# Kernel tuning notes

Hardware: AMD Instinct MI355X
Metric: run time of the kernel (lower is better)

The kernel has to match this reference:

```python
import jax, jax.numpy as jnp
import numpy as np

T, B = 512, 64
I, H, A, O = 256, 1024, 128, 1024  # input, hidden, adapt, output sizes


def _lstm_cell(x, h, c, wih, whh, bih, bhh):
    # standard torch nn.LSTMCell, gate order i,f,g,o
    g = x @ wih.T + bih + h @ whh.T + bhh
    i, f, gg, o = jnp.split(g, 4, axis=1)
    i = jax.nn.sigmoid(i)
    f = jax.nn.sigmoid(f)
    gg = jnp.tanh(gg)
    o = jax.nn.sigmoid(o)
    c2 = f * c + i * gg
    return o * jnp.tanh(c2), c2


def _alstm_cell(x, h, c, wih, whh, b, adapt, ninp, nhid):
    # adapt chunks: [ninp, nhid, 4*nhid, 4*nhid, 4*nhid]
    splits = [ninp, ninp + nhid, ninp + nhid + 4 * nhid, ninp + nhid + 8 * nhid]
    a_x, a_h, a_ig, a_hg, a_b = jnp.split(adapt, splits, axis=1)
    igates = ((x * a_x) @ wih.T) * a_ig + b * a_b
    hgates = ((h * a_h) @ whh.T) * a_hg
    g = igates + hgates
    i, f, gg, o = jnp.split(g, 4, axis=1)
    i = jax.nn.sigmoid(i)
    f = jax.nn.sigmoid(f)
    gg = jnp.tanh(gg)
    o = jax.nn.sigmoid(o)
    c2 = f * c + i * gg
    return o * jnp.tanh(c2), c2


def setup_inputs() -> dict:
    key = jax.random.key(0)
    ks = jax.random.split(key, 20)
    n = lambda k, *s: jax.random.normal(k, s, dtype=jnp.float32) * 0.05
    psz0 = I + 13 * H          # layer0 policy size
    psz1 = H + 13 * O          # layer1 policy size
    return {
        "x": jax.random.normal(ks[0], (T, B, I), dtype=jnp.float32),
        # layer 0 adapt LSTMCell: input = A + I + H
        "a_wih0": n(ks[1], 4 * A, A + I + H), "a_whh0": n(ks[2], 4 * A, A),
        "a_bih0": n(ks[3], 4 * A), "a_bhh0": n(ks[4], 4 * A),
        "p_w0": n(ks[5], psz0, A), "p_b0": n(ks[6], psz0),
        "f_wih0": n(ks[7], 4 * H, I), "f_whh0": n(ks[8], 4 * H, H), "f_b0": n(ks[9], 4 * H),
        # layer 1 (last): input = A + H + O
        "a_wih1": n(ks[10], 4 * A, A + H + O), "a_whh1": n(ks[11], 4 * A, A),
        "a_bih1": n(ks[12], 4 * A), "a_bhh1": n(ks[13], 4 * A),
        "p_w1": n(ks[14], psz1, A), "p_b1": n(ks[15], psz1),
        "f_wih1": n(ks[16], 4 * O, H), "f_whh1": n(ks[17], 4 * O, O), "f_b1": n(ks[18], 4 * O),
    }


def reference(x, a_wih0, a_whh0, a_bih0, a_bhh0, p_w0, p_b0, f_wih0, f_whh0, f_b0,
              a_wih1, a_whh1, a_bih1, a_bhh1, p_w1, p_b1, f_wih1, f_whh1, f_b1):
    bsz = x.shape[1]
    z = lambda n_: jnp.zeros((bsz, n_), x.dtype)

    def step(carry, xt):
        a0x, a0c, a1x, a1c, f0x, f0c, f1x, f1c = carry
        # layer 0: adapt input cats adapt_hidden[-1][0] == layer-1 adapt hx (prev t)
        ax0 = jnp.concatenate([xt, f0x, a1x], axis=1)
        a0x, a0c = _lstm_cell(ax0, a0x, a0c, a_wih0, a_whh0, a_bih0, a_bhh0)
        ahe0 = a0x @ p_w0.T + p_b0
        f0x, f0c = _alstm_cell(xt, f0x, f0c, f_wih0, f_whh0, f_b0, ahe0, I, H)
        # layer 1 (last): uses layer-0 adapt hx updated this step
        ax1 = jnp.concatenate([f0x, f1x, a0x], axis=1)
        a1x, a1c = _lstm_cell(ax1, a1x, a1c, a_wih1, a_whh1, a_bih1, a_bhh1)
        ahe1 = a1x @ p_w1.T + p_b1
        f1x, f1c = _alstm_cell(f0x, f1x, f1c, f_wih1, f_whh1, f_b1, ahe1, H, O)
        return (a0x, a0c, a1x, a1c, f0x, f0c, f1x, f1c), f1x

    init = (z(A), z(A), z(A), z(A), z(H), z(H), z(O), z(O))
    _, out = jax.lax.scan(step, init, x)  # out: [T, B, O]
    return out
```

## Files before the change

### kernel.cpp

```cpp
#include <hip/hip_runtime.h>

typedef __bf16 bf16x8 __attribute__((ext_vector_type(8)));
typedef float  f32x4  __attribute__((ext_vector_type(4)));

#define AS __HIP_MEMORY_SCOPE_AGENT

__device__ __forceinline__ float bf2f(unsigned short u) {
  union { unsigned int i; float f; } v; v.i = ((unsigned int)u) << 16; return v.f;
}
__device__ __forceinline__ unsigned short f2bf(float f) {
  union { float f; unsigned int u; } v; v.f = f;
  unsigned int r = v.u + 0x7fffu + ((v.u >> 16) & 1u);
  return (unsigned short)(r >> 16);
}
__device__ __forceinline__ float sigm(float x)   { return 1.f / (1.f + __expf(-x)); }
__device__ __forceinline__ float tanh_f(float x) { return 2.f / (1.f + __expf(-2.f * x)) - 1.f; }

__device__ __forceinline__ bf16x8 ld8(const unsigned short* p) {
  return *reinterpret_cast<const bf16x8*>(p);
}
__device__ __forceinline__ bf16x8 ldc8(const unsigned short* p) {
  const unsigned long long* q = (const unsigned long long*)p;
  union { unsigned long long u[2]; bf16x8 v; } r;
  r.u[0] = __hip_atomic_load(q + 0, __ATOMIC_RELAXED, AS);
  r.u[1] = __hip_atomic_load(q + 1, __ATOMIC_RELAXED, AS);
  return r.v;
}
__device__ __forceinline__ unsigned short ldc_bf(const unsigned short* p) {
  return __hip_atomic_load(p, __ATOMIC_RELAXED, AS);
}
__device__ __forceinline__ void stc_bf(unsigned short* p, unsigned short v) {
  __hip_atomic_store(p, v, __ATOMIC_RELAXED, AS);
}
__device__ __forceinline__ void stc2f(float* p, float a, float b) {
  union { float f[2]; unsigned long long u; } v; v.f[0] = a; v.f[1] = b;
  __hip_atomic_store((unsigned long long*)p, v.u, __ATOMIC_RELAXED, AS);
}
__device__ __forceinline__ void ldc2f(const float* p, float& a, float& b) {
  union { unsigned long long u; float f[2]; } v;
  v.u = __hip_atomic_load((const unsigned long long*)p, __ATOMIC_RELAXED, AS);
  a = v.f[0]; b = v.f[1];
}

__global__ __launch_bounds__(256) void f32_to_bf16(const float* __restrict__ src,
                                                   unsigned short* __restrict__ dst, int n4) {
  int i = blockIdx.x * blockDim.x + threadIdx.x;
  const int stride = gridDim.x * blockDim.x;
  const float4* s4 = (const float4*)src;
  ushort4* d4 = (ushort4*)dst;
  for (; i < n4; i += stride) {
    float4 v = s4[i];
    ushort4 o;
    o.x = f2bf(v.x); o.y = f2bf(v.y); o.z = f2bf(v.z); o.w = f2bf(v.w);
    d4[i] = o;
  }
}

struct SMem {
  unsigned short w1[16 * 64 * 32];
  unsigned short w0[10 * 64 * 32];
  f32x4 red_a[3][4][64];
};

#define G_BLOCKS 256
__device__ __forceinline__ void gbar(unsigned* bar, unsigned target) {
  asm volatile("s_waitcnt vmcnt(0)" ::: "memory");
  __syncthreads();
  if (threadIdx.x == 0) {
    __hip_atomic_fetch_add(bar, 1u, __ATOMIC_RELAXED, AS);
    while (__hip_atomic_load(bar, __ATOMIC_RELAXED, AS) < target) {
      __builtin_amdgcn_s_sleep(2);
    }
  }
  __syncthreads();
  asm volatile("" ::: "memory");
}

template<int XK, int HK>
__device__ __forceinline__ void preload(unsigned short* wl,
    const unsigned short* __restrict__ wih, const unsigned short* __restrict__ whh,
    int kq, int jb)
{
  constexpr int XC = XK / 32, CT = (XK + HK) / 32, CQ = CT / 4;
  const int c0 = kq * CQ, j0 = jb * 16;
  for (int it = threadIdx.x; it < CQ * 64; it += 256) {
    const int lc = it >> 6, r = it & 63;
    const int g = r >> 4, jj = r & 15;
    const int cg = c0 + lc;
    const unsigned short* src = (cg < XC)
        ? wih + (size_t)(g * 1024 + j0 + jj) * XK + cg * 32
        : whh + (size_t)(g * 1024 + j0 + jj) * HK + (cg - XC) * 32;
    ulonglong2* d = (ulonglong2*)(wl + (size_t)it * 32);
    const ulonglong2* s = (const ulonglong2*)src;
    d[0] = s[0]; d[1] = s[1]; d[2] = s[2]; d[3] = s[3];
  }
}

template<int C>
__device__ __forceinline__ void seg_quarter(f32x4 acc[4],
    const unsigned short* __restrict__ a, int astride,
    const unsigned short* __restrict__ w, int wstride,
    int m0, int j0, int quad, int col, int kq)
{
  constexpr int CQ = C / 4;
  const unsigned short* ar = a + (size_t)(m0 + col) * astride + quad * 8 + kq * CQ * 32;
  const unsigned short* wr = w + quad * 8 + kq * CQ * 32;
#pragma unroll
  for (int c = 0; c < CQ; c++) {
    bf16x8 af = ldc8(ar + c * 32);
#pragma unroll
    for (int g = 0; g < 4; g++) {
      acc[g] = __builtin_amdgcn_mfma_f32_16x16x32_bf16(
          af, ld8(wr + (size_t)(g * 128 + j0 + col) * wstride + c * 32),
          acc[g], 0, 0, 0);
    }
  }
}

template<int C0, int C1, int C2, int C3>
__device__ __forceinline__ void st_adapt(SMem& sm, int rel,
    const unsigned short* __restrict__ a0, int as0, const unsigned short* __restrict__ w0, int ws0,
    const unsigned short* __restrict__ a1, int as1, const unsigned short* __restrict__ w1, int ws1,
    const unsigned short* __restrict__ a2, int as2, const unsigned short* __restrict__ w2, int ws2,
    const unsigned short* __restrict__ a3, int as3, const unsigned short* __restrict__ w3, int ws3,
    const float* __restrict__ bih, const float* __restrict__ bhh,
    float* __restrict__ cbuf, unsigned short* __restrict__ hbuf)
{
  const int tid = threadIdx.x;
  const int kq = tid >> 6, lane = tid & 63;
  const int quad = lane >> 4, col = lane & 15;
  const int j0 = (rel & 7) * 16, m0 = (rel >> 3) * 16;

  f32x4 acc[4] = {};
  seg_quarter<C0>(acc, a0, as0, w0, ws0, m0, j0, quad, col, kq);
  seg_quarter<C1>(acc, a1, as1, w1, ws1, m0, j0, quad, col, kq);
  seg_quarter<C2>(acc, a2, as2, w2, ws2, m0, j0, quad, col, kq);
  seg_quarter<C3>(acc, a3, as3, w3, ws3, m0, j0, quad, col, kq);

  if (kq) {
#pragma unroll
    for (int g = 0; g < 4; g++) sm.red_a[kq - 1][g][lane] = acc[g];
  }
  __syncthreads();
  if (kq == 0) {
#pragma unroll
    for (int p = 0; p < 3; p++)
#pragma unroll
      for (int g = 0; g < 4; g++) acc[g] += sm.red_a[p][g][lane];

    const int j = j0 + col;
    const float b0 = bih[j]       + bhh[j];
    const float b1 = bih[128 + j] + bhh[128 + j];
    const float b2 = bih[256 + j] + bhh[256 + j];
    const float b3 = bih[384 + j] + bhh[384 + j];
#pragma unroll
    for (int r = 0; r < 4; r++) {
      const int m = m0 + quad * 4 + r;
      const float i_ = sigm(acc[0][r] + b0);
      const float f_ = sigm(acc[1][r] + b1);
      const float g_ = tanh_f(acc[2][r] + b2);
      const float o_ = sigm(acc[3][r] + b3);
      const int idx = m * 128 + j;
      const float c2 = f_ * cbuf[idx] + i_ * g_;
      cbuf[idx] = c2;
      stc_bf(&hbuf[idx], f2bf(o_ * tanh_f(c2)));
    }
  }
  __syncthreads();
}

__device__ __forceinline__ void st_policy(int blk,
    const unsigned short* __restrict__ A,
    const unsigned short* __restrict__ pw, const float* __restrict__ pb,
    const unsigned short* __restrict__ xsrc, int xn,
    const unsigned short* __restrict__ hsrc, int hn,
    unsigned short* __restrict__ xhat, unsigned short* __restrict__ hhat)
{
  const int wave = threadIdx.x >> 6, lane = threadIdx.x & 63;
  const int quad = lane >> 4, col = lane & 15;
  const int m0 = wave * 16, n0 = blk * 64;

  f32x4 acc[4] = {};
  const unsigned short* arow = A + (size_t)(m0 + col) * 128 + quad * 8;
#pragma unroll
  for (int c = 0; c < 4; c++) {
    bf16x8 af = ldc8(arow + c * 32);
#pragma unroll
    for (int s = 0; s < 4; s++) {
      acc[s] = __builtin_amdgcn_mfma_f32_16x16x32_bf16(
          af, ld8(pw + (size_t)(n0 + s * 16 + col) * 128 + quad * 8 + c * 32),
          acc[s], 0, 0, 0);
    }
  }
#pragma unroll
  for (int s = 0; s < 4; s++) {
    const int n = n0 + s * 16 + col;
    const float bias = pb[n];
#pragma unroll
    for (int r = 0; r < 4; r++) {
      const int m = m0 + quad * 4 + r;
      const float v = acc[s][r] + bias;
      if (n < xn) {
        stc_bf(&xhat[m * xn + n], f2bf(v * bf2f(ldc_bf(&xsrc[m * xn + n]))));
      } else {
        stc_bf(&hhat[m * hn + (n - xn)], f2bf(v * bf2f(ldc_bf(&hsrc[m * hn + (n - xn)]))));
      }
    }
  }
}

template<int XK, int HK>
__device__ __forceinline__ void st_fcell(SMem& sm, int jb, int kq,
    const unsigned short* __restrict__ xhat, const unsigned short* __restrict__ hhat,
    const float* __restrict__ fb, const unsigned short* __restrict__ ax,
    const unsigned short* __restrict__ pw, const float* __restrict__ pb,
    int ig_off, int hg_off, int ab_off,
    float* __restrict__ cbuf, unsigned short* __restrict__ hbuf, float* __restrict__ outp,
    float* __restrict__ pbuf, unsigned* fcnt, unsigned ftarget)
{
  constexpr int XC = XK / 32, CT = (XK + HK) / 32, CQ = CT / 4;
  const int tid = threadIdx.x;
  const int wave = tid >> 6, lane = tid & 63;
  const int quad = lane >> 4, col = lane & 15;
  const int m0 = wave * 16, j0 = jb * 16, c0 = kq * CQ;
  const unsigned short* wl = (XK == 1024) ? sm.w1 : sm.w0;

  f32x4 pg0[4] = {}, pg1[4] = {}, pg2[4] = {};
  if (kq == 0) {
    const unsigned short* ar = ax + (size_t)(m0 + col) * 128 + quad * 8;
#pragma unroll
    for (int c = 0; c < 4; c++) {
      bf16x8 af = ldc8(ar + c * 32);
#pragma unroll
      for (int g = 0; g < 4; g++) {
        pg0[g] = __builtin_amdgcn_mfma_f32_16x16x32_bf16(
            af, ld8(pw + (size_t)(ig_off + g * 1024 + j0 + col) * 128 + quad * 8 + c * 32), pg0[g], 0, 0, 0);
        pg1[g] = __builtin_amdgcn_mfma_f32_16x16x32_bf16(
            af, ld8(pw + (size_t)(hg_off + g * 1024 + j0 + col) * 128 + quad * 8 + c * 32), pg1[g], 0, 0, 0);
        pg2[g] = __builtin_amdgcn_mfma_f32_16x16x32_bf16(
            af, ld8(pw + (size_t)(ab_off + g * 1024 + j0 + col) * 128 + quad * 8 + c * 32), pg2[g], 0, 0, 0);
      }
    }
  }

  f32x4 ai[4] = {}, ah[4] = {};
#pragma unroll
  for (int lc = 0; lc < CQ; lc++) {
    const int cg = c0 + lc;
    const unsigned short* wr = wl + lc * 2048 + quad * 8;
    if (cg < XC) {
      bf16x8 af = ldc8(xhat + (size_t)(m0 + col) * XK + cg * 32 + quad * 8);
#pragma unroll
      for (int g = 0; g < 4; g++)
        ai[g] = __builtin_amdgcn_mfma_f32_16x16x32_bf16(af, ld8(wr + (g * 16 + col) * 32), ai[g], 0, 0, 0);
    } else {
      bf16x8 af = ldc8(hhat + (size_t)(m0 + col) * HK + (cg - XC) * 32 + quad * 8);
#pragma unroll
      for (int g = 0; g < 4; g++)
        ah[g] = __builtin_amdgcn_mfma_f32_16x16x32_bf16(af, ld8(wr + (g * 16 + col) * 32), ah[g], 0, 0, 0);
    }
  }

  if (kq) {
#pragma unroll
    for (int g = 0; g < 4; g++) {
      float* pi = pbuf + ((((((kq - 1) * 64 + jb) * 2 + 0) * 4 + wave) * 4 + g) * 64 + lane) * 4;
      float* ph = pbuf + ((((((kq - 1) * 64 + jb) * 2 + 1) * 4 + wave) * 4 + g) * 64 + lane) * 4;
      stc2f(pi, ai[g][0], ai[g][1]); stc2f(pi + 2, ai[g][2], ai[g][3]);
      stc2f(ph, ah[g][0], ah[g][1]); stc2f(ph + 2, ah[g][2], ah[g][3]);
    }
    asm volatile("s_waitcnt vmcnt(0)" ::: "memory");
    __syncthreads();
    if (tid == 0) __hip_atomic_fetch_add(&fcnt[jb], 1u, __ATOMIC_RELAXED, AS);
    return;
  }

  if (tid == 0) {
    while (__hip_atomic_load(&fcnt[jb], __ATOMIC_RELAXED, AS) < ftarget)
      __builtin_amdgcn_s_sleep(1);
  }
  __syncthreads();
  asm volatile("" ::: "memory");
#pragma unroll
  for (int kk = 0; kk < 3; kk++) {
#pragma unroll
    for (int g = 0; g < 4; g++) {
      const float* pi = pbuf + (((((kk * 64 + jb) * 2 + 0) * 4 + wave) * 4 + g) * 64 + lane) * 4;
      const float* ph = pbuf + (((((kk * 64 + jb) * 2 + 1) * 4 + wave) * 4 + g) * 64 + lane) * 4;
      float a, b, c, d;
      ldc2f(pi, a, b); ldc2f(pi + 2, c, d);
      ai[g][0] += a; ai[g][1] += b; ai[g][2] += c; ai[g][3] += d;
      ldc2f(ph, a, b); ldc2f(ph + 2, c, d);
      ah[g][0] += a; ah[g][1] += b; ah[g][2] += c; ah[g][3] += d;
    }
  }

  const int j = j0 + col;
  float pbi[4], pbh[4], pba[4], fbv[4];
#pragma unroll
  for (int g = 0; g < 4; g++) {
    pbi[g] = pb[ig_off + g * 1024 + j];
    pbh[g] = pb[hg_off + g * 1024 + j];
    pba[g] = pb[ab_off + g * 1024 + j];
    fbv[g] = fb[g * 1024 + j];
  }
#pragma unroll
  for (int r = 0; r < 4; r++) {
    const int m = m0 + quad * 4 + r;
    float gate[4];
#pragma unroll
    for (int g = 0; g < 4; g++) {
      gate[g] = ai[g][r] * (pg0[g][r] + pbi[g])
              + ah[g][r] * (pg1[g][r] + pbh[g])
              + fbv[g]   * (pg2[g][r] + pba[g]);
    }
    const float i_ = sigm(gate[0]);
    const float f_ = sigm(gate[1]);
    const float g_ = tanh_f(gate[2]);
    const float o_ = sigm(gate[3]);
    const int idx = m * 1024 + j;
    const float c2 = f_ * cbuf[idx] + i_ * g_;
    cbuf[idx] = c2;
    const float h = o_ * tanh_f(c2);
    stc_bf(&hbuf[idx], f2bf(h));
    if (outp) __builtin_nontemporal_store(h, &outp[idx]);
  }
}

__global__ __launch_bounds__(256) void alstm_persistent(
    const unsigned short* __restrict__ xb, float* __restrict__ out,
    const unsigned short* __restrict__ a_wih0b, const unsigned short* __restrict__ a_whh0b,
    const float* __restrict__ a_bih0, const float* __restrict__ a_bhh0,
    const unsigned short* __restrict__ p_w0b, const float* __restrict__ p_b0,
    const unsigned short* __restrict__ f_wih0b, const unsigned short* __restrict__ f_whh0b,
    const float* __restrict__ f_b0,
    const unsigned short* __restrict__ a_wih1b, const unsigned short* __restrict__ a_whh1b,
    const float* __restrict__ a_bih1, const float* __restrict__ a_bhh1,
    const unsigned short* __restrict__ p_w1b, const float* __restrict__ p_b1,
    const unsigned short* __restrict__ f_wih1b, const unsigned short* __restrict__ f_whh1b,
    const float* __restrict__ f_b1,
    float* a0c, float* a1c, float* f0c, float* f1c,
    unsigned short* a0xA, unsigned short* a0xB,
    unsigned short* a1xA, unsigned short* a1xB,
    unsigned short* f0x, unsigned short* f1x,
    unsigned short* xh0, unsigned short* hh0,
    unsigned short* xh1, unsigned short* hh1,
    float* pbuf, unsigned* fcnt, unsigned* bar)
{
  __shared__ SMem sm;
  const int blk = blockIdx.x;
  const int jb = blk & 63, kq = blk >> 6;
  unsigned ep = 0, fc_ep = 0;

  preload<1024, 1024>(sm.w1, f_wih1b, f_whh1b, kq, jb);
  preload<256,  1024>(sm.w0, f_wih0b, f_whh0b, kq, jb);
  __syncthreads();

  if (blk >= 32 && blk < 64)
    st_adapt<8, 32, 4, 4>(sm, blk - 32,
        xb, 256, a_wih0b, 1408,
        f0x, 1024, a_wih0b + 256, 1408,
        a1xB, 128, a_wih0b + 1280, 1408,
        a0xB, 128, a_whh0b, 128,
        a_bih0, a_bhh0, a0c, a0xA);
  gbar(bar, ++ep * (unsigned)G_BLOCKS);
  if (kq == 3 && jb < 20)
    st_policy(jb, a0xA, p_w0b, p_b0, xb, 256, f0x, 1024, xh0, hh0);
  gbar(bar, ++ep * (unsigned)G_BLOCKS);

#pragma unroll 1
  for (int t = 0; t < 512; t++) {
    const unsigned short* xt1 = xb + (size_t)(t + 1) * 64 * 256;
    unsigned short* a0x_cur  = (t & 1) ? a0xB : a0xA;
    unsigned short* a0x_nxt  = (t & 1) ? a0xA : a0xB;
    unsigned short* a1x_cur  = (t & 1) ? a1xB : a1xA;
    unsigned short* a1x_prev = (t & 1) ? a1xA : a1xB;
    const bool more = (t + 1 < 512);

    fc_ep++;
    st_fcell<256, 1024>(sm, jb, kq, xh0, hh0, f_b0,
                        a0x_cur, p_w0b, p_b0, 1280, 5376, 9472,
                        f0c, f0x, (float*)nullptr, pbuf, fcnt, 3u * fc_ep);
    gbar(bar, ++ep * (unsigned)G_BLOCKS);

    if (blk < 32)
      st_adapt<32, 32, 4, 4>(sm, blk,
          f0x, 1024, a_wih1b, 2176,
          f1x, 1024, a_wih1b + 1024, 2176,
          a0x_cur, 128, a_wih1b + 2048, 2176,
          a1x_prev, 128, a_whh1b, 128,
          a_bih1, a_bhh1, a1c, a1x_cur);
    gbar(bar, ++ep * (unsigned)G_BLOCKS);

    if (blk < 32)
      st_policy(blk, a1x_cur, p_w1b, p_b1, f0x, 1024, f1x, 1024, xh1, hh1);
    else if (blk < 64 && more)
      st_adapt<8, 32, 4, 4>(sm, blk - 32,
          xt1, 256, a_wih0b, 1408,
          f0x, 1024, a_wih0b + 256, 1408,
          a1x_cur, 128, a_wih0b + 1280, 1408,
          a0x_cur, 128, a_whh0b, 128,
          a_bih0, a_bhh0, a0c, a0x_nxt);
    gbar(bar, ++ep * (unsigned)G_BLOCKS);

    fc_ep++;
    st_fcell<1024, 1024>(sm, jb, kq, xh1, hh1, f_b1,
                         a1x_cur, p_w1b, p_b1, 2048, 6144, 10240,
                         f1c, f1x, out + (size_t)t * 64 * 1024, pbuf, fcnt, 3u * fc_ep);
    if (kq == 3 && jb < 20 && more)
      st_policy(jb, a0x_nxt, p_w0b, p_b0, xt1, 256, f0x, 1024, xh0, hh0);
    gbar(bar, ++ep * (unsigned)G_BLOCKS);
  }
}

extern "C" void kernel_launch(void* const* d_in, const int* in_sizes, int n_in,
                              void* d_out, int out_size, void* d_ws, size_t ws_size,
                              hipStream_t stream)
{
  const float* x      = (const float*)d_in[0];
  const float* a_wih0 = (const float*)d_in[1];
  const float* a_whh0 = (const float*)d_in[2];
  const float* a_bih0 = (const float*)d_in[3];
  const float* a_bhh0 = (const float*)d_in[4];
  const float* p_w0   = (const float*)d_in[5];
  const float* p_b0   = (const float*)d_in[6];
  const float* f_wih0 = (const float*)d_in[7];
  const float* f_whh0 = (const float*)d_in[8];
  const float* f_b0   = (const float*)d_in[9];
  const float* a_wih1 = (const float*)d_in[10];
  const float* a_whh1 = (const float*)d_in[11];
  const float* a_bih1 = (const float*)d_in[12];
  const float* a_bhh1 = (const float*)d_in[13];
  const float* p_w1   = (const float*)d_in[14];
  const float* p_b1   = (const float*)d_in[15];
  const float* f_wih1 = (const float*)d_in[16];
  const float* f_whh1 = (const float*)d_in[17];
  const float* f_b1   = (const float*)d_in[18];
  float* out = (float*)d_out;

  char* p = (char*)d_ws;
  auto alloc = [&](size_t bytes) { char* r = p; p += (bytes + 255) & ~(size_t)255; return r; };

  unsigned* bar  = (unsigned*)alloc(256);
  unsigned* fcnt = (unsigned*)alloc(256);
  float* a0c = (float*)alloc(64 * 128 * 4);
  float* a1c = (float*)alloc(64 * 128 * 4);
  float* f0c = (float*)alloc(64 * 1024 * 4);
  float* f1c = (float*)alloc(64 * 1024 * 4);
  unsigned short* a0xA = (unsigned short*)alloc(64 * 128 * 2);
  unsigned short* a0xB = (unsigned short*)alloc(64 * 128 * 2);
  unsigned short* a1xA = (unsigned short*)alloc(64 * 128 * 2);
  unsigned short* a1xB = (unsigned short*)alloc(64 * 128 * 2);
  unsigned short* f0x  = (unsigned short*)alloc(64 * 1024 * 2);
  unsigned short* f1x  = (unsigned short*)alloc(64 * 1024 * 2);
  const size_t zero_bytes = (size_t)(p - (char*)d_ws);

  unsigned short* xh0 = (unsigned short*)alloc(64 * 256 * 2);
  unsigned short* hh0 = (unsigned short*)alloc(64 * 1024 * 2);
  unsigned short* xh1 = (unsigned short*)alloc(64 * 1024 * 2);
  unsigned short* hh1 = (unsigned short*)alloc(64 * 1024 * 2);
  float* pbuf = (float*)alloc((size_t)3 * 64 * 2 * 16 * 64 * 4 * 4);

  unsigned short* xb      = (unsigned short*)alloc((size_t)8388608 * 2);
  unsigned short* a_wih0b = (unsigned short*)alloc((size_t)720896 * 2);
  unsigned short* a_whh0b = (unsigned short*)alloc((size_t)65536 * 2);
  unsigned short* p_w0b   = (unsigned short*)alloc((size_t)1736704 * 2);
  unsigned short* f_wih0b = (unsigned short*)alloc((size_t)1048576 * 2);
  unsigned short* f_whh0b = (unsigned short*)alloc((size_t)4194304 * 2);
  unsigned short* a_wih1b = (unsigned short*)alloc((size_t)1114112 * 2);
  unsigned short* a_whh1b = (unsigned short*)alloc((size_t)65536 * 2);
  unsigned short* p_w1b   = (unsigned short*)alloc((size_t)1835008 * 2);
  unsigned short* f_wih1b = (unsigned short*)alloc((size_t)4194304 * 2);
  unsigned short* f_whh1b = (unsigned short*)alloc((size_t)4194304 * 2);

  hipMemsetAsync(d_ws, 0, zero_bytes, stream);

  auto conv = [&](const float* s, unsigned short* d, size_t n) {
    int n4 = (int)(n >> 2);
    int blocks = (n4 + 255) / 256; if (blocks > 1024) blocks = 1024;
    f32_to_bf16<<<blocks, 256, 0, stream>>>(s, d, n4);
  };
  conv(x,      xb,      8388608);
  conv(a_wih0, a_wih0b, 720896);
  conv(a_whh0, a_whh0b, 65536);
  conv(p_w0,   p_w0b,   1736704);
  conv(f_wih0, f_wih0b, 1048576);
  conv(f_whh0, f_whh0b, 4194304);
  conv(a_wih1, a_wih1b, 1114112);
  conv(a_whh1, a_whh1b, 65536);
  conv(p_w1,   p_w1b,   1835008);
  conv(f_wih1, f_wih1b, 4194304);
  conv(f_whh1, f_whh1b, 4194304);

  alstm_persistent<<<G_BLOCKS, 256, 0, stream>>>(
      xb, out,
      a_wih0b, a_whh0b, a_bih0, a_bhh0, p_w0b, p_b0, f_wih0b, f_whh0b, f_b0,
      a_wih1b, a_whh1b, a_bih1, a_bhh1, p_w1b, p_b1, f_wih1b, f_whh1b, f_b1,
      a0c, a1c, f0c, f1c, a0xA, a0xB, a1xA, a1xB, f0x, f1x,
      xh0, hh0, xh1, hh1, pbuf, fcnt, bar);
}
```

Measured before the change: 69.12 ms.

## Replace a grid barrier with a flag wait and pre-combine split-K partials

The global barrier between the layer-1 adapt stage and the policy/layer-0 adapt stage becomes a counter flag. Blocks 32-95 spin on it, so adapt runs on blocks 0-31 and the dependent work moves to a disjoint set of blocks. In the f-cell, every K-quarter block now computes its own ig/hg policy scaling and writes one combined partial instead of separate ai/ah partials. This halves split-K traffic at the cost of redundant policy MFMAs. Activation loads are also hoisted ahead of the MFMAs, the fcnt counters are padded onto separate lines, and launch bounds gain a min-blocks hint.

```diff
diff --git a/kernel.cpp b/kernel.cpp
--- a/kernel.cpp
+++ b/kernel.cpp
@@ -182,13 +182,15 @@
 
   f32x4 acc[4] = {};
   const unsigned short* arow = A + (size_t)(m0 + col) * 128 + quad * 8;
+  bf16x8 afs[4];
+#pragma unroll
+  for (int c = 0; c < 4; c++) afs[c] = ldc8(arow + c * 32);
 #pragma unroll
   for (int c = 0; c < 4; c++) {
-    bf16x8 af = ldc8(arow + c * 32);
 #pragma unroll
     for (int s = 0; s < 4; s++) {
       acc[s] = __builtin_amdgcn_mfma_f32_16x16x32_bf16(
-          af, ld8(pw + (size_t)(n0 + s * 16 + col) * 128 + quad * 8 + c * 32),
+          afs[c], ld8(pw + (size_t)(n0 + s * 16 + col) * 128 + quad * 8 + c * 32),
           acc[s], 0, 0, 0);
     }
   }
@@ -225,82 +227,98 @@
   const int m0 = wave * 16, j0 = jb * 16, c0 = kq * CQ;
   const unsigned short* wl = (XK == 1024) ? sm.w1 : sm.w0;
 
-  f32x4 pg0[4] = {}, pg1[4] = {}, pg2[4] = {};
-  if (kq == 0) {
+  bf16x8 axr[4];
+  {
     const unsigned short* ar = ax + (size_t)(m0 + col) * 128 + quad * 8;
 #pragma unroll
-    for (int c = 0; c < 4; c++) {
-      bf16x8 af = ldc8(ar + c * 32);
-#pragma unroll
-      for (int g = 0; g < 4; g++) {
-        pg0[g] = __builtin_amdgcn_mfma_f32_16x16x32_bf16(
-            af, ld8(pw + (size_t)(ig_off + g * 1024 + j0 + col) * 128 + quad * 8 + c * 32), pg0[g], 0, 0, 0);
-        pg1[g] = __builtin_amdgcn_mfma_f32_16x16x32_bf16(
-            af, ld8(pw + (size_t)(hg_off + g * 1024 + j0 + col) * 128 + quad * 8 + c * 32), pg1[g], 0, 0, 0);
-        pg2[g] = __builtin_amdgcn_mfma_f32_16x16x32_bf16(
-            af, ld8(pw + (size_t)(ab_off + g * 1024 + j0 + col) * 128 + quad * 8 + c * 32), pg2[g], 0, 0, 0);
-      }
-    }
-  }
-
-  f32x4 ai[4] = {}, ah[4] = {};
+    for (int c = 0; c < 4; c++) axr[c] = ldc8(ar + c * 32);
+  }
+  bf16x8 act[CQ];
 #pragma unroll
   for (int lc = 0; lc < CQ; lc++) {
     const int cg = c0 + lc;
-    const unsigned short* wr = wl + lc * 2048 + quad * 8;
+    act[lc] = (cg < XC)
+        ? ldc8(xhat + (size_t)(m0 + col) * XK + cg * 32 + quad * 8)
+        : ldc8(hhat + (size_t)(m0 + col) * HK + (cg - XC) * 32 + quad * 8);
+  }
+  f32x4 pg0[4] = {}, pg1[4] = {}, pg2[4] = {};
+#pragma unroll
+  for (int c = 0; c < 4; c++) {
+#pragma unroll
+    for (int g = 0; g < 4; g++) {
+      pg0[g] = __builtin_amdgcn_mfma_f32_16x16x32_bf16(
+          axr[c], ld8(pw + (size_t)(ig_off + g * 1024 + j0 + col) * 128 + quad * 8 + c * 32), pg0[g], 0, 0, 0);
+      pg1[g] = __builtin_amdgcn_mfma_f32_16x16x32_bf16(
+          axr[c], ld8(pw + (size_t)(hg_off + g * 1024 + j0 + col) * 128 + quad * 8 + c * 32), pg1[g], 0, 0, 0);
+    }
+    if (kq == 0) {
+#pragma unroll
+      for (int g = 0; g < 4; g++) {
+        pg2[g] = __builtin_amdgcn_mfma_f32_16x16x32_bf16(
+            axr[c], ld8(pw + (size_t)(ab_off + g * 1024 + j0 + col) * 128 + quad * 8 + c * 32), pg2[g], 0, 0, 0);
+      }
+    }
+  }
+  f32x4 ai[4] = {}, ah[4] = {};
+#pragma unroll
+  for (int lc = 0; lc < CQ; lc++) {
+    const int cg = c0 + lc;
+    const unsigned short* wr = wl + lc * 2048 + col * 32 + quad * 8;
     if (cg < XC) {
-      bf16x8 af = ldc8(xhat + (size_t)(m0 + col) * XK + cg * 32 + quad * 8);
 #pragma unroll
       for (int g = 0; g < 4; g++)
-        ai[g] = __builtin_amdgcn_mfma_f32_16x16x32_bf16(af, ld8(wr + (g * 16 + col) * 32), ai[g], 0, 0, 0);
+        ai[g] = __builtin_amdgcn_mfma_f32_16x16x32_bf16(act[lc], ld8(wr + g * 512), ai[g], 0, 0, 0);
     } else {
-      bf16x8 af = ldc8(hhat + (size_t)(m0 + col) * HK + (cg - XC) * 32 + quad * 8);
 #pragma unroll
       for (int g = 0; g < 4; g++)
-        ah[g] = __builtin_amdgcn_mfma_f32_16x16x32_bf16(af, ld8(wr + (g * 16 + col) * 32), ah[g], 0, 0, 0);
-    }
-  }
-
-  if (kq) {
-#pragma unroll
-    for (int g = 0; g < 4; g++) {
-      float* pi = pbuf + ((((((kq - 1) * 64 + jb) * 2 + 0) * 4 + wave) * 4 + g) * 64 + lane) * 4;
-      float* ph = pbuf + ((((((kq - 1) * 64 + jb) * 2 + 1) * 4 + wave) * 4 + g) * 64 + lane) * 4;
-      stc2f(pi, ai[g][0], ai[g][1]); stc2f(pi + 2, ai[g][2], ai[g][3]);
-      stc2f(ph, ah[g][0], ah[g][1]); stc2f(ph + 2, ah[g][2], ah[g][3]);
-    }
-    asm volatile("s_waitcnt vmcnt(0)" ::: "memory");
-    __syncthreads();
-    if (tid == 0) __hip_atomic_fetch_add(&fcnt[jb], 1u, __ATOMIC_RELAXED, AS);
-    return;
-  }
-
-  if (tid == 0) {
-    while (__hip_atomic_load(&fcnt[jb], __ATOMIC_RELAXED, AS) < ftarget)
-      __builtin_amdgcn_s_sleep(1);
-  }
-  __syncthreads();
-  asm volatile("" ::: "memory");
-#pragma unroll
-  for (int kk = 0; kk < 3; kk++) {
-#pragma unroll
-    for (int g = 0; g < 4; g++) {
-      const float* pi = pbuf + (((((kk * 64 + jb) * 2 + 0) * 4 + wave) * 4 + g) * 64 + lane) * 4;
-      const float* ph = pbuf + (((((kk * 64 + jb) * 2 + 1) * 4 + wave) * 4 + g) * 64 + lane) * 4;
-      float a, b, c, d;
-      ldc2f(pi, a, b); ldc2f(pi + 2, c, d);
-      ai[g][0] += a; ai[g][1] += b; ai[g][2] += c; ai[g][3] += d;
-      ldc2f(ph, a, b); ldc2f(ph + 2, c, d);
-      ah[g][0] += a; ah[g][1] += b; ah[g][2] += c; ah[g][3] += d;
-    }
-  }
-
+        ah[g] = __builtin_amdgcn_mfma_f32_16x16x32_bf16(act[lc], ld8(wr + g * 512), ah[g], 0, 0, 0);
+    }
+  }
   const int j = j0 + col;
-  float pbi[4], pbh[4], pba[4], fbv[4];
+  float pbi[4], pbh[4];
 #pragma unroll
   for (int g = 0; g < 4; g++) {
     pbi[g] = pb[ig_off + g * 1024 + j];
     pbh[g] = pb[hg_off + g * 1024 + j];
+  }
+  f32x4 comb[4];
+#pragma unroll
+  for (int g = 0; g < 4; g++)
+#pragma unroll
+    for (int r = 0; r < 4; r++)
+      comb[g][r] = ai[g][r] * (pg0[g][r] + pbi[g]) + ah[g][r] * (pg1[g][r] + pbh[g]);
+
+  if (kq) {
+#pragma unroll
+    for (int g = 0; g < 4; g++) {
+      float* pp = pbuf + ((size_t)(((kq - 1) * 64 + jb) * 4 + wave) * 4 + g) * 256 + lane * 4;
+      stc2f(pp, comb[g][0], comb[g][1]); stc2f(pp + 2, comb[g][2], comb[g][3]);
+    }
+    asm volatile("s_waitcnt vmcnt(0)" ::: "memory");
+    __syncthreads();
+    if (tid == 0) __hip_atomic_fetch_add(&fcnt[jb * 8], 1u, __ATOMIC_RELAXED, AS);
+    return;
+  }
+
+  if (tid == 0) {
+    while (__hip_atomic_load(&fcnt[jb * 8], __ATOMIC_RELAXED, AS) < ftarget)
+      __builtin_amdgcn_s_sleep(1);
+  }
+  __syncthreads();
+  asm volatile("" ::: "memory");
+#pragma unroll
+  for (int kk = 0; kk < 3; kk++) {
+#pragma unroll
+    for (int g = 0; g < 4; g++) {
+      const float* pp = pbuf + ((size_t)((kk * 64 + jb) * 4 + wave) * 4 + g) * 256 + lane * 4;
+      float a, b, c, d;
+      ldc2f(pp, a, b); ldc2f(pp + 2, c, d);
+      comb[g][0] += a; comb[g][1] += b; comb[g][2] += c; comb[g][3] += d;
+    }
+  }
+  float pba[4], fbv[4];
+#pragma unroll
+  for (int g = 0; g < 4; g++) {
     pba[g] = pb[ab_off + g * 1024 + j];
     fbv[g] = fb[g * 1024 + j];
   }
@@ -309,11 +327,8 @@
     const int m = m0 + quad * 4 + r;
     float gate[4];
 #pragma unroll
-    for (int g = 0; g < 4; g++) {
-      gate[g] = ai[g][r] * (pg0[g][r] + pbi[g])
-              + ah[g][r] * (pg1[g][r] + pbh[g])
-              + fbv[g]   * (pg2[g][r] + pba[g]);
-    }
+    for (int g = 0; g < 4; g++)
+      gate[g] = comb[g][r] + fbv[g] * (pg2[g][r] + pba[g]);
     const float i_ = sigm(gate[0]);
     const float f_ = sigm(gate[1]);
     const float g_ = tanh_f(gate[2]);
@@ -327,7 +342,7 @@
   }
 }
 
-__global__ __launch_bounds__(256) void alstm_persistent(
+__global__ __launch_bounds__(256, 1) void alstm_persistent(
     const unsigned short* __restrict__ xb, float* __restrict__ out,
     const unsigned short* __restrict__ a_wih0b, const unsigned short* __restrict__ a_whh0b,
     const float* __restrict__ a_bih0, const float* __restrict__ a_bhh0,
@@ -345,11 +360,12 @@
     unsigned short* f0x, unsigned short* f1x,
     unsigned short* xh0, unsigned short* hh0,
     unsigned short* xh1, unsigned short* hh1,
-    float* pbuf, unsigned* fcnt, unsigned* bar)
+    float* pbuf, unsigned* fcnt, unsigned* bar, unsigned* abar)
 {
   __shared__ SMem sm;
   const int blk = blockIdx.x;
   const int jb = blk & 63, kq = blk >> 6;
+  const int tid = threadIdx.x;
   unsigned ep = 0, fc_ep = 0;
 
   preload<1024, 1024>(sm.w1, f_wih1b, f_whh1b, kq, jb);
@@ -383,24 +399,33 @@
                         f0c, f0x, (float*)nullptr, pbuf, fcnt, 3u * fc_ep);
     gbar(bar, ++ep * (unsigned)G_BLOCKS);
 
-    if (blk < 32)
+    if (blk < 32) {
       st_adapt<32, 32, 4, 4>(sm, blk,
           f0x, 1024, a_wih1b, 2176,
           f1x, 1024, a_wih1b + 1024, 2176,
           a0x_cur, 128, a_wih1b + 2048, 2176,
           a1x_prev, 128, a_whh1b, 128,
           a_bih1, a_bhh1, a1c, a1x_cur);
-    gbar(bar, ++ep * (unsigned)G_BLOCKS);
-
-    if (blk < 32)
-      st_policy(blk, a1x_cur, p_w1b, p_b1, f0x, 1024, f1x, 1024, xh1, hh1);
-    else if (blk < 64 && more)
-      st_adapt<8, 32, 4, 4>(sm, blk - 32,
-          xt1, 256, a_wih0b, 1408,
-          f0x, 1024, a_wih0b + 256, 1408,
-          a1x_cur, 128, a_wih0b + 1280, 1408,
-          a0x_cur, 128, a_whh0b, 128,
-          a_bih0, a_bhh0, a0c, a0x_nxt);
+      asm volatile("s_waitcnt vmcnt(0)" ::: "memory");
+      __syncthreads();
+      if (tid == 0) __hip_atomic_fetch_add(abar, 1u, __ATOMIC_RELAXED, AS);
+    } else if (blk < 96) {
+      if (tid == 0) {
+        while (__hip_atomic_load(abar, __ATOMIC_RELAXED, AS) < 32u * (unsigned)(t + 1))
+          __builtin_amdgcn_s_sleep(2);
+      }
+      __syncthreads();
+      asm volatile("" ::: "memory");
+      if (blk < 64)
+        st_policy(blk - 32, a1x_cur, p_w1b, p_b1, f0x, 1024, f1x, 1024, xh1, hh1);
+      else if (more)
+        st_adapt<8, 32, 4, 4>(sm, blk - 64,
+            xt1, 256, a_wih0b, 1408,
+            f0x, 1024, a_wih0b + 256, 1408,
+            a1x_cur, 128, a_wih0b + 1280, 1408,
+            a0x_cur, 128, a_whh0b, 128,
+            a_bih0, a_bhh0, a0c, a0x_nxt);
+    }
     gbar(bar, ++ep * (unsigned)G_BLOCKS);
 
     fc_ep++;
@@ -442,7 +467,8 @@
   auto alloc = [&](size_t bytes) { char* r = p; p += (bytes + 255) & ~(size_t)255; return r; };
 
   unsigned* bar  = (unsigned*)alloc(256);
-  unsigned* fcnt = (unsigned*)alloc(256);
+  unsigned* abar = (unsigned*)alloc(256);
+  unsigned* fcnt = (unsigned*)alloc(64 * 8 * 4);
   float* a0c = (float*)alloc(64 * 128 * 4);
   float* a1c = (float*)alloc(64 * 128 * 4);
   float* f0c = (float*)alloc(64 * 1024 * 4);
@@ -459,7 +485,7 @@
   unsigned short* hh0 = (unsigned short*)alloc(64 * 1024 * 2);
   unsigned short* xh1 = (unsigned short*)alloc(64 * 1024 * 2);
   unsigned short* hh1 = (unsigned short*)alloc(64 * 1024 * 2);
-  float* pbuf = (float*)alloc((size_t)3 * 64 * 2 * 16 * 64 * 4 * 4);
+  float* pbuf = (float*)alloc((size_t)3 * 64 * 4 * 4 * 256 * 4);
 
   unsigned short* xb      = (unsigned short*)alloc((size_t)8388608 * 2);
   unsigned short* a_wih0b = (unsigned short*)alloc((size_t)720896 * 2);
@@ -497,5 +523,5 @@
       a_wih0b, a_whh0b, a_bih0, a_bhh0, p_w0b, p_b0, f_wih0b, f_whh0b, f_b0,
       a_wih1b, a_whh1b, a_bih1, a_bhh1, p_w1b, p_b1, f_wih1b, f_whh1b, f_b1,
       a0c, a1c, f0c, f1c, a0xA, a0xB, a1xA, a1xB, f0x, f1x,
-      xh0, hh0, xh1, hh1, pbuf, fcnt, bar);
-}
+      xh0, hh0, xh1, hh1, pbuf, fcnt, bar, abar);
+}
```

Measured after the change: 57.88 ms. 1.19x faster.
